# Kernel optimization log

Measured on AMD Instinct MI355X. Metric: run time of the kernel, lower is better.

Reference implementation:

```python
import jax, jax.numpy as jnp
import numpy as np

NUM_GRAPHS = 128
EPS = 1e-5  # torch BatchNorm1d default eps


def setup_inputs() -> dict:
    key = jax.random.key(0)
    ks = jax.random.split(key, 24)
    N, E, NHE = 50000, 800000, 50000
    NODE_RAW, HEDGE_RAW, H, HH, HOUT = 92, 40, 128, 128, 256
    s = 0.05
    inp = {
        "x": jax.random.normal(ks[0], (N, NODE_RAW), jnp.float32),
        "hedge_attrs": jax.random.normal(ks[1], (NHE, HEDGE_RAW), jnp.float32),
        "inter_relations_index": jax.random.randint(ks[2], (3, E), 0, N, jnp.int64),
        "batch": jax.random.randint(ks[3], (N,), 0, NUM_GRAPHS, jnp.int64),
        "num_nodes": N,
        # embed: Linear(92, h_dim)
        "embed_w": jax.random.normal(ks[4], (NODE_RAW, H), jnp.float32) * s,
        "embed_b": jax.random.normal(ks[5], (H,), jnp.float32) * s,
        # bembed: Linear(hedge_dim, hidden_hedge_dim)
        "bembed_w": jax.random.normal(ks[6], (HEDGE_RAW, HH), jnp.float32) * s,
        "bembed_b": jax.random.normal(ks[7], (HH,), jnp.float32) * s,
        # conv.lin_full_presplit: Linear(2H+HH, 2H)
        "lin_w": jax.random.normal(ks[8], (2 * H + HH, 2 * H), jnp.float32) * s,
        "lin_b": jax.random.normal(ks[9], (2 * H,), jnp.float32) * s,
        "bn1_g": jnp.ones((2 * H,), jnp.float32),
        "bn1_b": jnp.zeros((2 * H,), jnp.float32),
        "bn2_g": jnp.ones((H,), jnp.float32),
        "bn2_b": jnp.zeros((H,), jnp.float32),
        # learnable temperature of SoftmaxAggregation (init 1.0)
        "aggr_t": jnp.ones((), jnp.float32),
        "l1_w": jax.random.normal(ks[10], (H, HOUT), jnp.float32) * s,
        "l1_b": jax.random.normal(ks[11], (HOUT,), jnp.float32) * s,
        "out_w": jax.random.normal(ks[12], (HOUT, 1), jnp.float32) * s,
        "out_b": jax.random.normal(ks[13], (1,), jnp.float32) * s,
    }
    return inp


def _batchnorm(z, g, b):
    mu = z.mean(axis=0)
    var = z.var(axis=0)  # biased, matching torch training-mode normalization
    return (z - mu) * jax.lax.rsqrt(var + EPS) * g + b


def reference(x, hedge_attrs, inter_relations_index, batch, num_nodes,
              embed_w, embed_b, bembed_w, bembed_b, lin_w, lin_b,
              bn1_g, bn1_b, bn2_g, bn2_b, aggr_t, l1_w, l1_b, out_w, out_b):
    idx0 = inter_relations_index[0]
    idx1 = inter_relations_index[1]
    connect_feats = hedge_attrs @ bembed_w + bembed_b          # [NHE, HH]
    h = x @ embed_w + embed_b                                   # [N, H]

    # --- CHGInterConv ---
    origin = h[idx0]                                            # [E, H]
    connect = connect_feats[idx1]                               # [E, HH]
    remote = h[idx0]                                            # faithful to source (uses idx0)
    z = jnp.concatenate([origin, connect, remote], axis=1)      # [E, 2H+HH]
    z = z @ lin_w + lin_b                                       # [E, 2H]
    z = _batchnorm(z, bn1_g, bn1_b)
    z_f, z_c = jnp.split(z, 2, axis=-1)
    msg = jax.nn.sigmoid(z_f) * jax.nn.softplus(z_c)            # [E, H]

    # learned SoftmaxAggregation: per-node, per-channel segment softmax of t*msg
    alpha = msg * aggr_t
    m = jax.ops.segment_max(alpha, idx0, num_segments=num_nodes)
    m = jnp.where(jnp.isfinite(m), m, 0.0)                      # empty segments
    e = jnp.exp(alpha - m[idx0])
    denom = jax.ops.segment_sum(e, idx0, num_segments=num_nodes)
    w = e / (denom[idx0] + 1e-16)
    out = jax.ops.segment_sum(msg * w, idx0, num_segments=num_nodes)  # [N, H]

    out = _batchnorm(out, bn2_g, bn2_b)
    h = jax.nn.softplus(out + h)                                # residual + softplus

    # --- global mean pool over graphs ---
    counts = jax.ops.segment_sum(jnp.ones((num_nodes,), h.dtype), batch,
                                 num_segments=NUM_GRAPHS)
    pooled = jax.ops.segment_sum(h, batch, num_segments=NUM_GRAPHS)
    pooled = pooled / jnp.maximum(counts, 1.0)[:, None]         # [G, H]

    g = jax.nn.softplus(pooled @ l1_w + l1_b)                   # [G, HOUT]
    return g @ out_w + out_b                                    # [G, 1]
```

## Files before the change

kernel.cpp:

```cpp
#include <hip/hip_runtime.h>
#include <hip/hip_bf16.h>


#define EPS_BN 1e-5f
#define LOG2E 1.4426950408889634f
#define LN2   0.6931471805599453f

#define BIN_SH 8
#define BIN_CHUNK 4096

typedef __attribute__((ext_vector_type(8))) short bf16x8;
typedef __attribute__((ext_vector_type(4))) float f32x4;
typedef __attribute__((ext_vector_type(2))) float f32x2;

__device__ __forceinline__ float fexp2(float x) {
#if __has_builtin(__builtin_amdgcn_exp2f)
    return __builtin_amdgcn_exp2f(x);
#else
    return __expf(x * LN2);
#endif
}
__device__ __forceinline__ float flog2(float x) {
#if __has_builtin(__builtin_amdgcn_logf)
    return __builtin_amdgcn_logf(x);
#else
    return __logf(x) * LOG2E;
#endif
}
__device__ __forceinline__ float softplus_fast(float x) {
    return LN2 * flog2(1.f + fexp2(x * LOG2E));
}

__device__ __forceinline__ f32x2 pk_fma2(f32x2 a, f32x2 b, f32x2 c) {
#if __has_builtin(__builtin_elementwise_fma)
    return __builtin_elementwise_fma(a, b, c);
#else
    return (f32x2){fmaf(a.x, b.x, c.x), fmaf(a.y, b.y, c.y)};
#endif
}

__device__ __forceinline__ unsigned short f2bf(float f) {
    unsigned u = __float_as_uint(f);
    unsigned r = (u + 0x7fffu + ((u >> 16) & 1u)) >> 16;
    return (unsigned short)r;
}
__device__ __forceinline__ float bflo(unsigned u) { return __uint_as_float(u << 16); }
__device__ __forceinline__ float bfhi(unsigned u) { return __uint_as_float(u & 0xffff0000u); }
__device__ __forceinline__ float bfu16(unsigned short v) { return __uint_as_float(((unsigned)v) << 16); }
__device__ __forceinline__ unsigned pack2bf(float x, float y) {
    return (unsigned)f2bf(x) | ((unsigned)f2bf(y) << 16);
}

#if __has_builtin(__builtin_amdgcn_cvt_pk_f32_fp8) && __has_builtin(__builtin_amdgcn_cvt_pk_fp8_f32)
#define HW_FP8 1
#else
#define HW_FP8 0
#endif

__device__ __forceinline__ unsigned char f2fp8(float f) {
#if HW_FP8
    int r = __builtin_amdgcn_cvt_pk_fp8_f32(f, f, 0, false);
    return (unsigned char)(r & 0xff);
#else
    unsigned u = __float_as_uint(f);
    unsigned s = (u >> 24) & 0x80u;
    float af = fabsf(f);
    if (!(af >= 0.015625f)) {
        int m = (int)rintf(af * 512.f);
        if (m > 7) m = 7;
        return (unsigned char)(s | (unsigned)m);
    }
    if (af > 448.f) return (unsigned char)(s | 0x7e);
    unsigned au = __float_as_uint(af);
    unsigned r = au + 0x7ffffu + ((au >> 20) & 1u);
    int e8 = (int)(r >> 23) - 120;
    unsigned m = (r >> 20) & 7u;
    if (e8 > 15 || (e8 == 15 && m == 7)) return (unsigned char)(s | 0x7e);
    return (unsigned char)(s | ((unsigned)e8 << 3) | m);
#endif
}

__device__ __forceinline__ void fp8pair(unsigned p, f32x2& lo, f32x2& hi) {
#if HW_FP8
    lo = __builtin_amdgcn_cvt_pk_f32_fp8((int)p, false);
    hi = __builtin_amdgcn_cvt_pk_f32_fp8((int)p, true);
#else
    auto dec = [](unsigned byte) -> float {
        unsigned s = (byte & 0x80u) << 24;
        unsigned em = byte & 0x7fu;
        float nrm = __uint_as_float(s | ((em << 20) + 0x3C000000u));
        float sub = __uint_as_float(s | 0x3F800000u) * (float)em * 0.001953125f;
        return (em >= 8) ? nrm : sub;
    };
    lo = (f32x2){dec(p & 0xff), dec((p >> 8) & 0xff)};
    hi = (f32x2){dec((p >> 16) & 0xff), dec(p >> 24)};
#endif
}

__device__ __forceinline__ int perm256(int j) {
    return (j < 128) ? ((j >> 1) * 4 + (j & 1)) : (((j - 128) >> 1) * 4 + 2 + (j & 1));
}

__global__ __launch_bounds__(256) void k_prepw(const float* __restrict__ ew, const float* __restrict__ bw,
                                               const float* __restrict__ lw,
                                               unsigned short* __restrict__ embB, unsigned short* __restrict__ bembB,
                                               unsigned short* __restrict__ waB, unsigned short* __restrict__ wcB) {
    int i = blockIdx.x * 256 + threadIdx.x;
    if (i >= 81920) return;
    unsigned short* dst;
    int f, NKC, CT, mode;
    if (i < 12288)      { dst = embB;  f = i;         NKC = 3; CT = 2; mode = 0; }
    else if (i < 20480) { dst = bembB; f = i - 12288; NKC = 2; CT = 2; mode = 1; }
    else if (i < 53248) { dst = waB;   f = i - 20480; NKC = 4; CT = 4; mode = 2; }
    else                { dst = wcB;   f = i - 53248; NKC = 4; CT = 4; mode = 3; }
    int j = f & 7, l = (f >> 3) & 63;
    int r2 = f >> 9;
    int c = r2 % CT;
    int r3 = r2 / CT;
    int kc = r3 % NKC, w = r3 / NKC;
    int k = kc * 32 + ((l >> 4) & 3) * 8 + j;
    int n = (w * CT + c) * 16 + (l & 15);
    float v;
    if (mode == 0)      v = (k < 92) ? ew[k * 128 + n] : 0.f;
    else if (mode == 1) v = (k < 40) ? bw[k * 128 + n] : 0.f;
    else if (mode == 2) v = lw[k * 256 + n] + lw[(k + 256) * 256 + n];
    else                v = lw[(k + 128) * 256 + n];
    dst[f] = f2bf(v);
}

template<int KIN, int NKC1, int OMODE2>
__global__ __launch_bounds__(256) void mfma_fused(
    const float* __restrict__ in, const unsigned short* __restrict__ B1, const float* __restrict__ bias1,
    const unsigned short* __restrict__ B2, const float* __restrict__ bias2,
    unsigned short* __restrict__ hout, void* __restrict__ out2, int M,
    const int* __restrict__ aux_idx, int* __restrict__ aux_hist, int aux_cnt)
{
    const int r0 = blockIdx.x * 32;
    const int t = threadIdx.x;
    const int w = t >> 6;
    const int l = t & 63;
    const int m = l & 15, q = l >> 4;

    if (aux_idx) {
        const int T = gridDim.x * 256;
        for (int i = blockIdx.x * 256 + t; i < aux_cnt; i += T)
            atomicAdd(&aux_hist[aux_idx[i]], 1);
    }

    __shared__ __align__(16) unsigned short als[32 * NKC1 * 32];
    __shared__ __align__(16) unsigned short hls[32 * 136];

    const int KP = NKC1 * 32;
    for (int i = t; i < 32 * KP; i += 256) {
        int r = i / KP, k = i - r * KP;
        int gr = r0 + r;
        float v = (gr < M && k < KIN) ? in[(size_t)gr * KIN + k] : 0.f;
        int idx = (((r >> 4) * NKC1 + (k >> 5)) * 64 + ((k >> 3) & 3) * 16 + (r & 15)) * 8 + (k & 7);
        als[idx] = f2bf(v);
    }
    bf16x8 b1[NKC1][2];
    const bf16x8* B1f = (const bf16x8*)B1;
#pragma unroll
    for (int kc = 0; kc < NKC1; kc++)
#pragma unroll
        for (int c = 0; c < 2; c++)
            b1[kc][c] = B1f[((w * NKC1 + kc) * 2 + c) * 64 + l];
    __syncthreads();

    f32x4 acc1[2][2];
#pragma unroll
    for (int c = 0; c < 2; c++) { acc1[c][0] = (f32x4){0.f,0.f,0.f,0.f}; acc1[c][1] = (f32x4){0.f,0.f,0.f,0.f}; }
    const bf16x8* af = (const bf16x8*)als;
#pragma unroll
    for (int kc = 0; kc < NKC1; kc++) {
        bf16x8 a0 = af[kc * 64 + l];
        bf16x8 a1 = af[(NKC1 + kc) * 64 + l];
#pragma unroll
        for (int c = 0; c < 2; c++) {
            acc1[c][0] = __builtin_amdgcn_mfma_f32_16x16x32_bf16(a0, b1[kc][c], acc1[c][0], 0, 0, 0);
            acc1[c][1] = __builtin_amdgcn_mfma_f32_16x16x32_bf16(a1, b1[kc][c], acc1[c][1], 0, 0, 0);
        }
    }
#pragma unroll
    for (int c = 0; c < 2; c++) {
        int n1 = (w * 2 + c) * 16 + m;
        float bv = bias1[n1];
#pragma unroll
        for (int hh = 0; hh < 2; hh++) {
#pragma unroll
            for (int r = 0; r < 4; r++) {
                int row = hh * 16 + q * 4 + r;
                float val = acc1[c][hh][r] + bv;
                unsigned short bf = f2bf(val);
                hls[row * 136 + n1] = bf;
                if (OMODE2 == 1 && r0 + row < M) hout[(size_t)(r0 + row) * 128 + n1] = bf;
            }
        }
    }
    __syncthreads();

    bf16x8 b2[4][4];
    const bf16x8* B2f = (const bf16x8*)B2;
#pragma unroll
    for (int kc = 0; kc < 4; kc++)
#pragma unroll
        for (int c = 0; c < 4; c++)
            b2[kc][c] = B2f[((w * 4 + kc) * 4 + c) * 64 + l];

    f32x4 acc2[4][2];
#pragma unroll
    for (int c = 0; c < 4; c++) { acc2[c][0] = (f32x4){0.f,0.f,0.f,0.f}; acc2[c][1] = (f32x4){0.f,0.f,0.f,0.f}; }
#pragma unroll
    for (int kc = 0; kc < 4; kc++) {
        bf16x8 a0 = *(const bf16x8*)(hls + m * 136 + kc * 32 + q * 8);
        bf16x8 a1 = *(const bf16x8*)(hls + (m + 16) * 136 + kc * 32 + q * 8);
#pragma unroll
        for (int c = 0; c < 4; c++) {
            acc2[c][0] = __builtin_amdgcn_mfma_f32_16x16x32_bf16(a0, b2[kc][c], acc2[c][0], 0, 0, 0);
            acc2[c][1] = __builtin_amdgcn_mfma_f32_16x16x32_bf16(a1, b2[kc][c], acc2[c][1], 0, 0, 0);
        }
    }
#pragma unroll
    for (int c = 0; c < 4; c++) {
        int n = (w * 4 + c) * 16 + m;
        float bv = bias2 ? bias2[n] : 0.f;
        int pj = perm256(n);
#pragma unroll
        for (int hh = 0; hh < 2; hh++) {
#pragma unroll
            for (int r = 0; r < 4; r++) {
                int row = r0 + hh * 16 + q * 4 + r;
                if (row < M) {
                    float val = acc2[c][hh][r] + bv;
                    if (OMODE2 == 1) ((unsigned short*)out2)[(size_t)row * 256 + pj] = f2bf(val);
                    else             ((unsigned char*)out2)[(size_t)row * 256 + pj] = f2fp8(val);
                }
            }
        }
    }
}

__global__ __launch_bounds__(256) void k_count(const int* __restrict__ idx0, int* __restrict__ bsum,
                                               int E, int NB) {
    __shared__ int lhist[256];
    const int t = threadIdx.x;
    const int e0 = blockIdx.x * BIN_CHUNK;
    const int cnt = min(E - e0, BIN_CHUNK);
    lhist[t] = 0;
    __syncthreads();
    for (int i = t; i < cnt; i += 256)
        atomicAdd(&lhist[idx0[e0 + i] >> BIN_SH], 1);
    __syncthreads();
    if (t < NB && lhist[t]) atomicAdd(&bsum[t], lhist[t]);
}

__global__ __launch_bounds__(256) void k_scanB(const int* __restrict__ bsum, int* __restrict__ boff,
                                               const int* __restrict__ gcount, int* __restrict__ gptr, int NB) {
    __shared__ int s[256];
    const int t = threadIdx.x;
    int v = (t < NB) ? bsum[t] : 0;
    s[t] = v;
    __syncthreads();
#pragma unroll
    for (int ofs = 1; ofs < 256; ofs <<= 1) {
        int u = (t >= ofs) ? s[t - ofs] : 0;
        __syncthreads();
        s[t] += u;
        __syncthreads();
    }
    if (t < NB) boff[t] = s[t] - v;
    if (t == NB - 1) boff[NB] = s[t];
    __syncthreads();
    int gv = (t < 128) ? gcount[t] : 0;
    s[t] = gv;
    __syncthreads();
#pragma unroll
    for (int ofs = 1; ofs < 128; ofs <<= 1) {
        int u = (t >= ofs && t < 128) ? s[t - ofs] : 0;
        __syncthreads();
        if (t < 128) s[t] += u;
        __syncthreads();
    }
    if (t < 128) gptr[t + 1] = s[t];
    if (t == 0) gptr[0] = 0;
}

__global__ __launch_bounds__(256) void k_binA(
    const int* __restrict__ idx0, const int* __restrict__ idx1,
    const int* __restrict__ boff, int* __restrict__ bfill,
    int* __restrict__ staging,
    const int* __restrict__ batch, const int* __restrict__ gptr,
    int* __restrict__ gfill, int* __restrict__ gnodes,
    int E, int N, int NB, int EB)
{
    const int t = threadIdx.x;
    const int bid = blockIdx.x;
    if (bid >= EB) {
        int i = (bid - EB) * 256 + t;
        if (i < N) {
            int g = batch[i];
            int pos = gptr[g] + atomicAdd(&gfill[g], 1);
            gnodes[pos] = i;
        }
        return;
    }
    __shared__ int svals[BIN_CHUNK];
    __shared__ unsigned char sbk[BIN_CHUNK];
    __shared__ int lhist[256], lbase[256];
    const int e0 = bid * BIN_CHUNK;
    const int cnt = min(E - e0, BIN_CHUNK);
    for (int b = t; b < NB; b += 256) lhist[b] = 0;
    __syncthreads();
    for (int i = t; i < cnt; i += 256) {
        int n = idx0[e0 + i];
        int m = idx1[e0 + i];
        int bk = n >> BIN_SH;
        sbk[i] = (unsigned char)bk;
        svals[i] = (m << BIN_SH) | (n & ((1 << BIN_SH) - 1));
        atomicAdd(&lhist[bk], 1);
    }
    __syncthreads();
    for (int b = t; b < NB; b += 256) {
        int h = lhist[b];
        int base = h ? atomicAdd(&bfill[b], h) : 0;
        lbase[b] = boff[b] + base;
        lhist[b] = 0;
    }
    __syncthreads();
    for (int i = t; i < cnt; i += 256) {
        int bk = sbk[i];
        int r = atomicAdd(&lhist[bk], 1);
        staging[lbase[bk] + r] = svals[i];
    }
}

__global__ __launch_bounds__(256) void k_binB(
    const int* __restrict__ boff, const int* __restrict__ staging,
    int* __restrict__ rowptr, int* __restrict__ sidx1, int E, int N)
{
    __shared__ int lcnt[256];
    __shared__ int noofs[256];
    __shared__ int s[256];
    const int t = threadIdx.x;
    const int b = blockIdx.x;
    const int n0 = b << BIN_SH;
    const int nn = min(N - n0, 256);
    const int s0 = boff[b], s1 = boff[b + 1];
    lcnt[t] = 0;
    __syncthreads();
    for (int i = s0 + t; i < s1; i += 256)
        atomicAdd(&lcnt[staging[i] & 255], 1);
    __syncthreads();
    int v = lcnt[t];
    s[t] = v;
    __syncthreads();
#pragma unroll
    for (int ofs = 1; ofs < 256; ofs <<= 1) {
        int u = (t >= ofs) ? s[t - ofs] : 0;
        __syncthreads();
        s[t] += u;
        __syncthreads();
    }
    noofs[t] = s[t] - v;
    if (t < nn) rowptr[n0 + t] = s0 + s[t] - v;
    lcnt[t] = 0;
    if (b == 0 && t == 0) rowptr[N] = E;
    __syncthreads();
    for (int i = s0 + t; i < s1; i += 256) {
        int vv = staging[i];
        int nl = vv & 255;
        int r = atomicAdd(&lcnt[nl], 1);
        sidx1[s0 + noofs[nl] + r] = vv & 0xffffff00;
    }
}

__global__ __launch_bounds__(256) void k_stats(const uint2* __restrict__ A16, const unsigned char* __restrict__ Cp8b,
                                               const int* __restrict__ rowptr, const int* __restrict__ sidx1,
                                               float* __restrict__ gsum, float* __restrict__ gsq,
                                               int E, int N, int per_slot) {
    __shared__ float4 lsm4[256], lsq4[256];
    const int t = threadIdx.x;
    const int l = t & 63;
    const int wid = __builtin_amdgcn_readfirstlane(t >> 6);
    const int slot = blockIdx.x * 4 + wid;
    const unsigned lo4 = (unsigned)(l << 2);
    const long base = (long)slot * per_slot;
    const int e0 = (int)min((long)E, base);
    const int e1 = (int)min((long)E, base + per_slot);
    f32x2 smF = {0.f,0.f}, smC = {0.f,0.f};
    f32x2 sqF = {0.f,0.f}, sqC = {0.f,0.f};
    f32x2 csrF = {0.f,0.f}, csrC = {0.f,0.f};
    f32x2 aF = {0.f,0.f}, aC = {0.f,0.f};
    int cur_n = 0, bound = 0, runk = 0;

    auto flush = [&]() {
        if (runk) {
            float fk = (float)runk;
            f32x2 fk2 = {fk, fk};
            smF += csrF; smC += csrC;
            smF = pk_fma2(fk2, aF, smF);
            smC = pk_fma2(fk2, aC, smC);
            f32x2 tF = pk_fma2(fk2, aF, csrF + csrF);
            f32x2 tC = pk_fma2(fk2, aC, csrC + csrC);
            sqF = pk_fma2(aF, tF, sqF);
            sqC = pk_fma2(aC, tC, sqC);
        }
        csrF = (f32x2){0.f,0.f}; csrC = (f32x2){0.f,0.f};
        runk = 0;
    };
    auto loadA = [&](int n) {
        uint2 a8 = A16[(size_t)n * 64 + l];
        aF = (f32x2){bflo(a8.x), bfhi(a8.x)};
        aC = (f32x2){bflo(a8.y), bfhi(a8.y)};
    };

    if (e0 < e1) {
        int lo = 0, hi = N;
        while (lo + 1 < hi) {
            int mid = (lo + hi) >> 1;
            int rv = __builtin_amdgcn_readfirstlane(rowptr[mid]);
            if (rv <= e0) lo = mid; else hi = mid;
        }
        cur_n = lo;
        bound = __builtin_amdgcn_readfirstlane(rowptr[cur_n + 1]);
        loadA(cur_n);
    }

    auto proc = [&](int e, unsigned p) {
        if (e >= bound) {
            flush();
            do { cur_n++; bound = __builtin_amdgcn_readfirstlane(rowptr[cur_n + 1]); } while (bound <= e);
            loadA(cur_n);
        }
        f32x2 vf, vc;
        fp8pair(p, vf, vc);
        csrF += vf; csrC += vc;
        sqF = pk_fma2(vf, vf, sqF);
        sqC = pk_fma2(vc, vc, sqC);
        runk++;
    };

    const int nfull = (e1 - e0) & ~7;
    if (nfull > 0) {
        int eg = e0;
        unsigned cur[8];
        {
            int4 m0 = *(const int4*)(sidx1 + eg);
            int4 m1 = *(const int4*)(sidx1 + eg + 4);
            cur[0] = *(const unsigned*)(Cp8b + ((unsigned)m0.x + lo4));
            cur[1] = *(const unsigned*)(Cp8b + ((unsigned)m0.y + lo4));
            cur[2] = *(const unsigned*)(Cp8b + ((unsigned)m0.z + lo4));
            cur[3] = *(const unsigned*)(Cp8b + ((unsigned)m0.w + lo4));
            cur[4] = *(const unsigned*)(Cp8b + ((unsigned)m1.x + lo4));
            cur[5] = *(const unsigned*)(Cp8b + ((unsigned)m1.y + lo4));
            cur[6] = *(const unsigned*)(Cp8b + ((unsigned)m1.z + lo4));
            cur[7] = *(const unsigned*)(Cp8b + ((unsigned)m1.w + lo4));
        }
        for (;;) {
            const int en = eg + 8;
            const bool more = en < e0 + nfull;
            unsigned nxt[8];
            if (more) {
                int4 t0 = *(const int4*)(sidx1 + en);
                int4 t1 = *(const int4*)(sidx1 + en + 4);
                nxt[0] = *(const unsigned*)(Cp8b + ((unsigned)t0.x + lo4));
                nxt[1] = *(const unsigned*)(Cp8b + ((unsigned)t0.y + lo4));
                nxt[2] = *(const unsigned*)(Cp8b + ((unsigned)t0.z + lo4));
                nxt[3] = *(const unsigned*)(Cp8b + ((unsigned)t0.w + lo4));
                nxt[4] = *(const unsigned*)(Cp8b + ((unsigned)t1.x + lo4));
                nxt[5] = *(const unsigned*)(Cp8b + ((unsigned)t1.y + lo4));
                nxt[6] = *(const unsigned*)(Cp8b + ((unsigned)t1.z + lo4));
                nxt[7] = *(const unsigned*)(Cp8b + ((unsigned)t1.w + lo4));
            }
            proc(eg, cur[0]);     proc(eg + 1, cur[1]);
            proc(eg + 2, cur[2]); proc(eg + 3, cur[3]);
            proc(eg + 4, cur[4]); proc(eg + 5, cur[5]);
            proc(eg + 6, cur[6]); proc(eg + 7, cur[7]);
            if (!more) break;
#pragma unroll
            for (int i = 0; i < 8; i++) cur[i] = nxt[i];
            eg = en;
        }
    }
    for (int e = e0 + nfull; e < e1; e++)
        proc(e, *(const unsigned*)(Cp8b + ((unsigned)sidx1[e] + lo4)));
    flush();

    lsm4[t] = (float4){smF.x, smF.y, smC.x, smC.y};
    lsq4[t] = (float4){sqF.x, sqF.y, sqC.x, sqC.y};
    __syncthreads();
    const float* fm = (const float*)lsm4;
    const float* fq = (const float*)lsq4;
    float vs = fm[t] + fm[256 + t] + fm[512 + t] + fm[768 + t];
    float vq = fq[t] + fq[256 + t] + fq[512 + t] + fq[768 + t];
    atomicAdd(&gsum[t], vs);
    atomicAdd(&gsq[t], vq);
}

__global__ __launch_bounds__(256) void k_aggr(const uint2* __restrict__ A16, const unsigned char* __restrict__ Cp8b,
                                              const int* __restrict__ rowptr, const int* __restrict__ sidx1,
                                              const float* __restrict__ bn1_sum, const float* __restrict__ bn1_sq,
                                              const float* __restrict__ g1, const float* __restrict__ b1,
                                              const float* __restrict__ tptr, unsigned* __restrict__ out,
                                              float invE, int N) {
    const int t = threadIdx.x;
    const int l = t & 63;
    const int wid = __builtin_amdgcn_readfirstlane(t >> 6);
    const int n = blockIdx.x * 4 + wid;
    if (n >= N) return;

    const int e0 = __builtin_amdgcn_readfirstlane(rowptr[n]);
    const int e1 = __builtin_amdgcn_readfirstlane(rowptr[n + 1]);

    const float tt = tptr[0];
    const float4 sum4 = ((const float4*)bn1_sum)[l];
    const float4 sq4  = ((const float4*)bn1_sq)[l];
    const float2 gf = ((const float2*)g1)[l];
    const float2 gc = ((const float2*)(g1 + 128))[l];
    const float2 bf2 = ((const float2*)b1)[l];
    const float2 bc2 = ((const float2*)(b1 + 128))[l];
    auto mkss = [&](float sum, float sq, float gg, float bb, float& sc, float& sh) {
        float mu = sum * invE;
        float var = sq * invE - mu * mu;
        sc = gg * rsqrtf(var + EPS_BN);
        sh = fmaf(-mu, sc, bb);
    };
    float scx, shx, scy, shy, scz, shz, scw, shw;
    mkss(sum4.x, sq4.x, gf.x, bf2.x, scx, shx);
    mkss(sum4.y, sq4.y, gf.y, bf2.y, scy, shy);
    mkss(sum4.z, sq4.z, gc.x, bc2.x, scz, shz);
    mkss(sum4.w, sq4.w, gc.y, bc2.y, scw, shw);
    const f32x2 sF  = {-scx * LOG2E, -scy * LOG2E};
    const f32x2 sC  = { scz * LOG2E,  scw * LOG2E};

    uint2 a8 = A16[(size_t)n * 64 + l];
    f32x2 aF = {bflo(a8.x), bfhi(a8.x)}, aC = {bflo(a8.y), bfhi(a8.y)};
    const f32x2 bF = pk_fma2(aF, sF, (f32x2){-shx * LOG2E, -shy * LOG2E});
    const f32x2 bC = pk_fma2(aC, sC, (f32x2){ shz * LOG2E,  shw * LOG2E});

    if (e0 >= e1) { out[(size_t)n * 64 + l] = 0u; return; }

    const unsigned lo4 = (unsigned)(l << 2);
    f32x2 den = {0.f,0.f}, num = {0.f,0.f};

    auto G = [&](int e) -> unsigned {
        return *(const unsigned*)(Cp8b + ((unsigned)sidx1[e] + lo4));
    };
    auto procg = [&](unsigned p) {
        f32x2 vf, vc;
        fp8pair(p, vf, vc);
        f32x2 argf = pk_fma2(vf, sF, bF);
        f32x2 argc = pk_fma2(vc, sC, bC);
        f32x2 ef = {fexp2(argf.x), fexp2(argf.y)};
        f32x2 uu = {fexp2(argc.x), fexp2(argc.y)};
        f32x2 d1 = ef + 1.f;
        f32x2 u1 = uu + 1.f;
        f32x2 sig = {__builtin_amdgcn_rcpf(d1.x), __builtin_amdgcn_rcpf(d1.y)};
        f32x2 lg = {flog2(u1.x), flog2(u1.y)};
        f32x2 M = sig * lg;
        f32x2 tM = M * tt;
        f32x2 w = {fexp2(tM.x), fexp2(tM.y)};
        den += w;
        num = pk_fma2(M, w, num);
    };

    const int cnt = e1 - e0;
    unsigned cur[8];
#pragma unroll
    for (int i = 0; i < 8; i++)
        if (i < cnt) cur[i] = G(e0 + i);

    int e = e0;
    while (e + 8 < e1) {
        unsigned nxt[8];
#pragma unroll
        for (int i = 0; i < 8; i++)
            if (e + 8 + i < e1) nxt[i] = G(e + 8 + i);
#pragma unroll
        for (int i = 0; i < 8; i++) procg(cur[i]);
#pragma unroll
        for (int i = 0; i < 8; i++) cur[i] = nxt[i];
        e += 8;
    }
    const int rem = e1 - e;
#pragma unroll
    for (int i = 0; i < 8; i++)
        if (i < rem) procg(cur[i]);

    float ox = LN2 * num.x * __builtin_amdgcn_rcpf(den.x);
    float oy = LN2 * num.y * __builtin_amdgcn_rcpf(den.y);
    out[(size_t)n * 64 + l] = pack2bf(ox, oy);
}

__global__ __launch_bounds__(256) void k_bn2stats(const unsigned* __restrict__ outw, float* __restrict__ sum,
                                                  float* __restrict__ sq, int N) {
    __shared__ float4 ls[256];
    const int t = threadIdx.x;
    const int w = t & 63;
    const int rg = t >> 6;
    f32x2 sm = {0.f,0.f}, s2 = {0.f,0.f};
    for (int n = blockIdx.x * 4 + rg; n < N; n += gridDim.x * 4) {
        unsigned v = outw[(size_t)n * 64 + w];
        f32x2 x = {bflo(v), bfhi(v)};
        sm += x;
        s2 = pk_fma2(x, x, s2);
    }
    ls[t] = (float4){sm.x, sm.y, s2.x, s2.y};
    __syncthreads();
    if (t < 64) {
        float4 a = ls[t], b = ls[t + 64], c = ls[t + 128], d = ls[t + 192];
        atomicAdd(&sum[2 * w],     a.x + b.x + c.x + d.x);
        atomicAdd(&sum[2 * w + 1], a.y + b.y + c.y + d.y);
        atomicAdd(&sq[2 * w],      a.z + b.z + c.z + d.z);
        atomicAdd(&sq[2 * w + 1],  a.w + b.w + c.w + d.w);
    }
}

template<int SPLIT>
__global__ __launch_bounds__(128) void k_h2pool(const unsigned short* __restrict__ out,
                                                const unsigned short* __restrict__ h,
                                                const int* __restrict__ gptr, const int* __restrict__ gnodes,
                                                const float* __restrict__ bn2_sum, const float* __restrict__ bn2_sq,
                                                const float* __restrict__ g2, const float* __restrict__ b2,
                                                float* __restrict__ pooled, float invN) {
    const int g = blockIdx.x & 127;
    const int sp = blockIdx.x >> 7;
    const int c = threadIdx.x;
    float mu = bn2_sum[c] * invN;
    float var = bn2_sq[c] * invN - mu * mu;
    float sc = g2[c] * rsqrtf(var + EPS_BN);
    float sh = fmaf(-mu, sc, b2[c]);
    const int i0 = gptr[g], i1 = gptr[g + 1];
    float acc = 0.f;
    for (int i = i0 + sp; i < i1; i += SPLIT) {
        int n = gnodes[i];
        float v = fmaf(bfu16(out[(size_t)n * 128 + c]), sc, sh) + bfu16(h[(size_t)n * 128 + c]);
        acc += softplus_fast(v);
    }
    if (acc != 0.f) atomicAdd(&pooled[g * 128 + c], acc);
}

__global__ __launch_bounds__(256) void k_head(const float* __restrict__ pooled, const int* __restrict__ gcount,
                                              const float* __restrict__ l1w, const float* __restrict__ l1b,
                                              const float* __restrict__ outw, const float* __restrict__ outb,
                                              float* __restrict__ dout) {
    __shared__ float p[128];
    __shared__ float red[256];
    const int g = blockIdx.x;
    const int j = threadIdx.x;
    if (j < 128) {
        float cnt = (float)max(gcount[g], 1);
        p[j] = pooled[g * 128 + j] / cnt;
    }
    __syncthreads();
    float acc = l1b[j];
    for (int k = 0; k < 128; k++) acc = fmaf(p[k], l1w[k * 256 + j], acc);
    red[j] = softplus_fast(acc) * outw[j];
    __syncthreads();
    for (int s = 128; s > 0; s >>= 1) {
        if (j < s) red[j] += red[j + s];
        __syncthreads();
    }
    if (j == 0) dout[g] = red[0] + outb[0];
}

extern "C" void kernel_launch(void* const* d_in, const int* in_sizes, int n_in,
                              void* d_out, int out_size, void* d_ws, size_t ws_size,
                              hipStream_t stream) {
    const float* x        = (const float*)d_in[0];
    const float* hedge    = (const float*)d_in[1];
    const int*   iri      = (const int*)d_in[2];
    const int*   batch    = (const int*)d_in[3];
    const float* embed_w  = (const float*)d_in[5];
    const float* embed_b  = (const float*)d_in[6];
    const float* bembed_w = (const float*)d_in[7];
    const float* bembed_b = (const float*)d_in[8];
    const float* lin_w    = (const float*)d_in[9];
    const float* lin_b    = (const float*)d_in[10];
    const float* bn1_g    = (const float*)d_in[11];
    const float* bn1_b    = (const float*)d_in[12];
    const float* bn2_g    = (const float*)d_in[13];
    const float* bn2_b    = (const float*)d_in[14];
    const float* aggr_t   = (const float*)d_in[15];
    const float* l1_w     = (const float*)d_in[16];
    const float* l1_b     = (const float*)d_in[17];
    const float* out_w    = (const float*)d_in[18];
    const float* out_b    = (const float*)d_in[19];

    const int N   = in_sizes[0] / 92;
    const int NHE = in_sizes[1] / 40;
    const int E   = in_sizes[2] / 3;
    const int* idx0 = iri;
    const int* idx1 = iri + E;

    float* ws = (float*)d_ws;
    size_t off = 0;
    auto alloc = [&](size_t elems) -> float* {
        float* p = ws + off;
        off += (elems + 63) & ~(size_t)63;
        return p;
    };
    unsigned short* h16 = (unsigned short*)alloc((size_t)N * 64);
    uint2* A16    = (uint2*)alloc((size_t)N * 128);
    unsigned* Cp8 = (unsigned*)alloc((size_t)NHE * 64);
    unsigned short* embB  = (unsigned short*)alloc(6144);
    unsigned short* bembB = (unsigned short*)alloc(4096);
    unsigned short* waB   = (unsigned short*)alloc(16384);
    unsigned short* wcB   = (unsigned short*)alloc(16384);
    int*   rowptr = (int*)alloc((size_t)N + 1);
    int*   boff   = (int*)alloc(260);
    int*   sidx1  = (int*)alloc((size_t)E + 8);
    int*   staging = (int*)alloc((size_t)E + 8);
    int*   gptr   = (int*)alloc(129);
    int*   gnodes = (int*)alloc((size_t)N);
    unsigned* outbuf = (unsigned*)alloc((size_t)N * 64);
    float* zbase  = ws + off;
    int*   bsum   = (int*)alloc(256);
    int*   bfill  = (int*)alloc(256);
    int*   gfill  = (int*)alloc(128);
    float* bn1_sum = alloc(256);
    float* bn1_sq  = alloc(256);
    float* bn2_sum = alloc(128);
    float* bn2_sq  = alloc(128);
    float* pooled  = alloc(128 * 128);
    int*   gcount  = (int*)alloc(128);
    size_t zbytes = (size_t)((ws + off) - zbase) * sizeof(float);
    (void)ws_size;

    hipMemsetAsync(zbase, 0, zbytes, stream);

    k_prepw<<<320, 256, 0, stream>>>(embed_w, bembed_w, lin_w, embB, bembB, waB, wcB);
    const int mtN   = (N + 31) / 32;
    const int mtNHE = (NHE + 31) / 32;
    mfma_fused<92, 3, 1><<<mtN, 256, 0, stream>>>(x, embB, embed_b, waB, lin_b, h16, A16, N,
                                                  nullptr, nullptr, 0);
    mfma_fused<40, 2, 2><<<mtNHE, 256, 0, stream>>>(hedge, bembB, bembed_b, wcB, nullptr, nullptr, Cp8, NHE,
                                                    batch, gcount, N);

    const int NB = (N + 255) >> BIN_SH;
    const int EB = (E + BIN_CHUNK - 1) / BIN_CHUNK;
    k_count<<<EB, 256, 0, stream>>>(idx0, bsum, E, NB);
    k_scanB<<<1, 256, 0, stream>>>(bsum, boff, gcount, gptr, NB);

    const int GB = (N + 255) / 256;
    k_binA<<<EB + GB, 256, 0, stream>>>(idx0, idx1, boff, bfill, staging,
                                        batch, gptr, gfill, gnodes, E, N, NB, EB);

    k_binB<<<NB, 256, 0, stream>>>(boff, staging, rowptr, sidx1, E, N);

    const int EDGE_BLOCKS = 2048;
    const int NSLOTS = EDGE_BLOCKS * 4;
    int per_slot = ((E + NSLOTS - 1) / NSLOTS + 7) & ~7;
    k_stats<<<EDGE_BLOCKS, 256, 0, stream>>>(A16, (const unsigned char*)Cp8, rowptr, sidx1,
                                             bn1_sum, bn1_sq, E, N, per_slot);

    k_aggr<<<(N + 3) / 4, 256, 0, stream>>>(A16, (const unsigned char*)Cp8, rowptr, sidx1,
                                            bn1_sum, bn1_sq, bn1_g, bn1_b, aggr_t, outbuf,
                                            1.0f / (float)E, N);

    k_bn2stats<<<256, 256, 0, stream>>>((const unsigned*)outbuf, bn2_sum, bn2_sq, N);
    k_h2pool<16><<<128 * 16, 128, 0, stream>>>((const unsigned short*)outbuf, h16, gptr, gnodes,
                                               bn2_sum, bn2_sq, bn2_g, bn2_b, pooled, 1.0f / (float)N);

    k_head<<<128, 256, 0, stream>>>(pooled, gcount, l1_w, l1_b, out_w, out_b, (float*)d_out);
}
```

Before: 444.8 us.

## Store node outputs in graph-sorted order and precompute edge slot start nodes

Node-level outputs (h16 and the aggregation buffer) are now written at graph-sorted positions computed by a new scatter kernel. The pooling kernel can then read contiguous rows instead of gathering through a node list. The edge-bin and batch histograms move into the weight-prep kernel, and the k_count kernel is removed. k_binB now precomputes each stats slot's starting node, so k_stats no longer binary-searches rowptr. This trades scattered writes in the GEMM and aggregation kernels, plus an extra launch, for coalesced pooling reads and fewer searches.

```diff
diff --git a/kernel.cpp b/kernel.cpp
--- a/kernel.cpp
+++ b/kernel.cpp
@@ -101,11 +101,36 @@
     return (j < 128) ? ((j >> 1) * 4 + (j & 1)) : (((j - 128) >> 1) * 4 + 2 + (j & 1));
 }
 
-__global__ __launch_bounds__(256) void k_prepw(const float* __restrict__ ew, const float* __restrict__ bw,
-                                               const float* __restrict__ lw,
-                                               unsigned short* __restrict__ embB, unsigned short* __restrict__ bembB,
-                                               unsigned short* __restrict__ waB, unsigned short* __restrict__ wcB) {
-    int i = blockIdx.x * 256 + threadIdx.x;
+__global__ __launch_bounds__(256) void k_pre(const float* __restrict__ ew, const float* __restrict__ bw,
+                                             const float* __restrict__ lw,
+                                             unsigned short* __restrict__ embB, unsigned short* __restrict__ bembB,
+                                             unsigned short* __restrict__ waB, unsigned short* __restrict__ wcB,
+                                             const int* __restrict__ idx0, const int* __restrict__ batch,
+                                             int* __restrict__ bsum, int* __restrict__ gcount,
+                                             int E, int N, int NB) {
+    const int t = threadIdx.x;
+    const int bid = blockIdx.x;
+    if (bid >= 320) {
+        __shared__ int lhist[256];
+        __shared__ int lbat[128];
+        const int cb = bid - 320;
+        lhist[t] = 0;
+        if (t < 128) lbat[t] = 0;
+        __syncthreads();
+        const int e0 = cb * BIN_CHUNK;
+        const int ecnt = min(E - e0, BIN_CHUNK);
+        for (int i = t; i < ecnt; i += 256)
+            atomicAdd(&lhist[idx0[e0 + i] >> BIN_SH], 1);
+        const int n0 = cb * BIN_CHUNK;
+        const int ncnt = min(N - n0, BIN_CHUNK);
+        for (int i = t; i < ncnt; i += 256)
+            atomicAdd(&lbat[batch[n0 + i]], 1);
+        __syncthreads();
+        if (t < NB && lhist[t]) atomicAdd(&bsum[t], lhist[t]);
+        if (t < 128 && lbat[t]) atomicAdd(&gcount[t], lbat[t]);
+        return;
+    }
+    int i = bid * 256 + t;
     if (i >= 81920) return;
     unsigned short* dst;
     int f, NKC, CT, mode;
@@ -128,24 +153,58 @@
     dst[f] = f2bf(v);
 }
 
+__global__ __launch_bounds__(256) void k_scanB(const int* __restrict__ bsum, int* __restrict__ boff,
+                                               const int* __restrict__ gcount, int* __restrict__ gptr, int NB) {
+    __shared__ int s[256];
+    const int t = threadIdx.x;
+    int v = (t < NB) ? bsum[t] : 0;
+    s[t] = v;
+    __syncthreads();
+#pragma unroll
+    for (int ofs = 1; ofs < 256; ofs <<= 1) {
+        int u = (t >= ofs) ? s[t - ofs] : 0;
+        __syncthreads();
+        s[t] += u;
+        __syncthreads();
+    }
+    if (t < NB) boff[t] = s[t] - v;
+    if (t == NB - 1) boff[NB] = s[t];
+    __syncthreads();
+    int gv = (t < 128) ? gcount[t] : 0;
+    s[t] = gv;
+    __syncthreads();
+#pragma unroll
+    for (int ofs = 1; ofs < 128; ofs <<= 1) {
+        int u = (t >= ofs && t < 128) ? s[t - ofs] : 0;
+        __syncthreads();
+        if (t < 128) s[t] += u;
+        __syncthreads();
+    }
+    if (t < 128) gptr[t + 1] = s[t];
+    if (t == 0) gptr[0] = 0;
+}
+
+__global__ __launch_bounds__(256) void k_scatterpos(const int* __restrict__ batch, const int* __restrict__ gptr,
+                                                    int* __restrict__ gfill, int* __restrict__ pos_of, int N) {
+    int i = blockIdx.x * 256 + threadIdx.x;
+    if (i < N) {
+        int g = batch[i];
+        pos_of[i] = gptr[g] + atomicAdd(&gfill[g], 1);
+    }
+}
+
 template<int KIN, int NKC1, int OMODE2>
 __global__ __launch_bounds__(256) void mfma_fused(
     const float* __restrict__ in, const unsigned short* __restrict__ B1, const float* __restrict__ bias1,
     const unsigned short* __restrict__ B2, const float* __restrict__ bias2,
     unsigned short* __restrict__ hout, void* __restrict__ out2, int M,
-    const int* __restrict__ aux_idx, int* __restrict__ aux_hist, int aux_cnt)
+    const int* __restrict__ pos_of)
 {
     const int r0 = blockIdx.x * 32;
     const int t = threadIdx.x;
     const int w = t >> 6;
     const int l = t & 63;
     const int m = l & 15, q = l >> 4;
-
-    if (aux_idx) {
-        const int T = gridDim.x * 256;
-        for (int i = blockIdx.x * 256 + t; i < aux_cnt; i += T)
-            atomicAdd(&aux_hist[aux_idx[i]], 1);
-    }
 
     __shared__ __align__(16) unsigned short als[32 * NKC1 * 32];
     __shared__ __align__(16) unsigned short hls[32 * 136];
@@ -193,7 +252,8 @@
                 float val = acc1[c][hh][r] + bv;
                 unsigned short bf = f2bf(val);
                 hls[row * 136 + n1] = bf;
-                if (OMODE2 == 1 && r0 + row < M) hout[(size_t)(r0 + row) * 128 + n1] = bf;
+                if (OMODE2 == 1 && r0 + row < M)
+                    hout[(size_t)pos_of[r0 + row] * 128 + n1] = bf;
             }
         }
     }
@@ -240,70 +300,13 @@
     }
 }
 
-__global__ __launch_bounds__(256) void k_count(const int* __restrict__ idx0, int* __restrict__ bsum,
-                                               int E, int NB) {
-    __shared__ int lhist[256];
-    const int t = threadIdx.x;
-    const int e0 = blockIdx.x * BIN_CHUNK;
-    const int cnt = min(E - e0, BIN_CHUNK);
-    lhist[t] = 0;
-    __syncthreads();
-    for (int i = t; i < cnt; i += 256)
-        atomicAdd(&lhist[idx0[e0 + i] >> BIN_SH], 1);
-    __syncthreads();
-    if (t < NB && lhist[t]) atomicAdd(&bsum[t], lhist[t]);
-}
-
-__global__ __launch_bounds__(256) void k_scanB(const int* __restrict__ bsum, int* __restrict__ boff,
-                                               const int* __restrict__ gcount, int* __restrict__ gptr, int NB) {
-    __shared__ int s[256];
-    const int t = threadIdx.x;
-    int v = (t < NB) ? bsum[t] : 0;
-    s[t] = v;
-    __syncthreads();
-#pragma unroll
-    for (int ofs = 1; ofs < 256; ofs <<= 1) {
-        int u = (t >= ofs) ? s[t - ofs] : 0;
-        __syncthreads();
-        s[t] += u;
-        __syncthreads();
-    }
-    if (t < NB) boff[t] = s[t] - v;
-    if (t == NB - 1) boff[NB] = s[t];
-    __syncthreads();
-    int gv = (t < 128) ? gcount[t] : 0;
-    s[t] = gv;
-    __syncthreads();
-#pragma unroll
-    for (int ofs = 1; ofs < 128; ofs <<= 1) {
-        int u = (t >= ofs && t < 128) ? s[t - ofs] : 0;
-        __syncthreads();
-        if (t < 128) s[t] += u;
-        __syncthreads();
-    }
-    if (t < 128) gptr[t + 1] = s[t];
-    if (t == 0) gptr[0] = 0;
-}
-
 __global__ __launch_bounds__(256) void k_binA(
     const int* __restrict__ idx0, const int* __restrict__ idx1,
     const int* __restrict__ boff, int* __restrict__ bfill,
-    int* __restrict__ staging,
-    const int* __restrict__ batch, const int* __restrict__ gptr,
-    int* __restrict__ gfill, int* __restrict__ gnodes,
-    int E, int N, int NB, int EB)
+    int* __restrict__ staging, int E, int NB)
 {
     const int t = threadIdx.x;
     const int bid = blockIdx.x;
-    if (bid >= EB) {
-        int i = (bid - EB) * 256 + t;
-        if (i < N) {
-            int g = batch[i];
-            int pos = gptr[g] + atomicAdd(&gfill[g], 1);
-            gnodes[pos] = i;
-        }
-        return;
-    }
     __shared__ int svals[BIN_CHUNK];
     __shared__ unsigned char sbk[BIN_CHUNK];
     __shared__ int lhist[256], lbase[256];
@@ -336,7 +339,8 @@
 
 __global__ __launch_bounds__(256) void k_binB(
     const int* __restrict__ boff, const int* __restrict__ staging,
-    int* __restrict__ rowptr, int* __restrict__ sidx1, int E, int N)
+    int* __restrict__ rowptr, int* __restrict__ sidx1, int* __restrict__ slots,
+    int E, int N, int per_slot)
 {
     __shared__ int lcnt[256];
     __shared__ int noofs[256];
@@ -366,6 +370,19 @@
     lcnt[t] = 0;
     if (b == 0 && t == 0) rowptr[N] = E;
     __syncthreads();
+    if (s1 > s0) {
+        int sfirst = (s0 + per_slot - 1) / per_slot;
+        int slast  = (s1 - 1) / per_slot;
+        for (int si = sfirst + t; si <= slast; si += 256) {
+            int tgt = si * per_slot - s0;
+            int lo = 0, hi = nn;
+            while (lo + 1 < hi) {
+                int mid = (lo + hi) >> 1;
+                if (noofs[mid] <= tgt) lo = mid; else hi = mid;
+            }
+            slots[si] = n0 + lo;
+        }
+    }
     for (int i = s0 + t; i < s1; i += 256) {
         int vv = staging[i];
         int nl = vv & 255;
@@ -376,6 +393,7 @@
 
 __global__ __launch_bounds__(256) void k_stats(const uint2* __restrict__ A16, const unsigned char* __restrict__ Cp8b,
                                                const int* __restrict__ rowptr, const int* __restrict__ sidx1,
+                                               const int* __restrict__ slots,
                                                float* __restrict__ gsum, float* __restrict__ gsq,
                                                int E, int N, int per_slot) {
     __shared__ float4 lsm4[256], lsq4[256];
@@ -415,13 +433,7 @@
     };
 
     if (e0 < e1) {
-        int lo = 0, hi = N;
-        while (lo + 1 < hi) {
-            int mid = (lo + hi) >> 1;
-            int rv = __builtin_amdgcn_readfirstlane(rowptr[mid]);
-            if (rv <= e0) lo = mid; else hi = mid;
-        }
-        cur_n = lo;
+        cur_n = __builtin_amdgcn_readfirstlane(slots[slot]);
         bound = __builtin_amdgcn_readfirstlane(rowptr[cur_n + 1]);
         loadA(cur_n);
     }
@@ -499,6 +511,7 @@
 
 __global__ __launch_bounds__(256) void k_aggr(const uint2* __restrict__ A16, const unsigned char* __restrict__ Cp8b,
                                               const int* __restrict__ rowptr, const int* __restrict__ sidx1,
+                                              const int* __restrict__ pos_of,
                                               const float* __restrict__ bn1_sum, const float* __restrict__ bn1_sq,
                                               const float* __restrict__ g1, const float* __restrict__ b1,
                                               const float* __restrict__ tptr, unsigned* __restrict__ out,
@@ -511,6 +524,7 @@
 
     const int e0 = __builtin_amdgcn_readfirstlane(rowptr[n]);
     const int e1 = __builtin_amdgcn_readfirstlane(rowptr[n + 1]);
+    const int pn = __builtin_amdgcn_readfirstlane(pos_of[n]);
 
     const float tt = tptr[0];
     const float4 sum4 = ((const float4*)bn1_sum)[l];
@@ -538,7 +552,7 @@
     const f32x2 bF = pk_fma2(aF, sF, (f32x2){-shx * LOG2E, -shy * LOG2E});
     const f32x2 bC = pk_fma2(aC, sC, (f32x2){ shz * LOG2E,  shw * LOG2E});
 
-    if (e0 >= e1) { out[(size_t)n * 64 + l] = 0u; return; }
+    if (e0 >= e1) { out[(size_t)pn * 64 + l] = 0u; return; }
 
     const unsigned lo4 = (unsigned)(l << 2);
     f32x2 den = {0.f,0.f}, num = {0.f,0.f};
@@ -589,7 +603,7 @@
 
     float ox = LN2 * num.x * __builtin_amdgcn_rcpf(den.x);
     float oy = LN2 * num.y * __builtin_amdgcn_rcpf(den.y);
-    out[(size_t)n * 64 + l] = pack2bf(ox, oy);
+    out[(size_t)pn * 64 + l] = pack2bf(ox, oy);
 }
 
 __global__ __launch_bounds__(256) void k_bn2stats(const unsigned* __restrict__ outw, float* __restrict__ sum,
@@ -619,7 +633,7 @@
 template<int SPLIT>
 __global__ __launch_bounds__(128) void k_h2pool(const unsigned short* __restrict__ out,
                                                 const unsigned short* __restrict__ h,
-                                                const int* __restrict__ gptr, const int* __restrict__ gnodes,
+                                                const int* __restrict__ gptr,
                                                 const float* __restrict__ bn2_sum, const float* __restrict__ bn2_sq,
                                                 const float* __restrict__ g2, const float* __restrict__ b2,
                                                 float* __restrict__ pooled, float invN) {
@@ -633,8 +647,7 @@
     const int i0 = gptr[g], i1 = gptr[g + 1];
     float acc = 0.f;
     for (int i = i0 + sp; i < i1; i += SPLIT) {
-        int n = gnodes[i];
-        float v = fmaf(bfu16(out[(size_t)n * 128 + c]), sc, sh) + bfu16(h[(size_t)n * 128 + c]);
+        float v = fmaf(bfu16(out[(size_t)i * 128 + c]), sc, sh) + bfu16(h[(size_t)i * 128 + c]);
         acc += softplus_fast(v);
     }
     if (acc != 0.f) atomicAdd(&pooled[g * 128 + c], acc);
@@ -712,54 +725,53 @@
     int*   sidx1  = (int*)alloc((size_t)E + 8);
     int*   staging = (int*)alloc((size_t)E + 8);
     int*   gptr   = (int*)alloc(129);
-    int*   gnodes = (int*)alloc((size_t)N);
+    int*   pos_of = (int*)alloc((size_t)N);
+    int*   slots  = (int*)alloc(8200);
     unsigned* outbuf = (unsigned*)alloc((size_t)N * 64);
     float* zbase  = ws + off;
     int*   bsum   = (int*)alloc(256);
     int*   bfill  = (int*)alloc(256);
     int*   gfill  = (int*)alloc(128);
+    int*   gcount = (int*)alloc(128);
     float* bn1_sum = alloc(256);
     float* bn1_sq  = alloc(256);
     float* bn2_sum = alloc(128);
     float* bn2_sq  = alloc(128);
     float* pooled  = alloc(128 * 128);
-    int*   gcount  = (int*)alloc(128);
     size_t zbytes = (size_t)((ws + off) - zbase) * sizeof(float);
     (void)ws_size;
 
     hipMemsetAsync(zbase, 0, zbytes, stream);
 
-    k_prepw<<<320, 256, 0, stream>>>(embed_w, bembed_w, lin_w, embB, bembB, waB, wcB);
+    const int NB = (N + 255) >> BIN_SH;
+    const int EB = (E + BIN_CHUNK - 1) / BIN_CHUNK;
+
+    k_pre<<<320 + EB, 256, 0, stream>>>(embed_w, bembed_w, lin_w, embB, bembB, waB, wcB,
+                                        idx0, batch, bsum, gcount, E, N, NB);
+    k_scanB<<<1, 256, 0, stream>>>(bsum, boff, gcount, gptr, NB);
+    k_scatterpos<<<(N + 255) / 256, 256, 0, stream>>>(batch, gptr, gfill, pos_of, N);
+
     const int mtN   = (N + 31) / 32;
     const int mtNHE = (NHE + 31) / 32;
-    mfma_fused<92, 3, 1><<<mtN, 256, 0, stream>>>(x, embB, embed_b, waB, lin_b, h16, A16, N,
-                                                  nullptr, nullptr, 0);
+    mfma_fused<92, 3, 1><<<mtN, 256, 0, stream>>>(x, embB, embed_b, waB, lin_b, h16, A16, N, pos_of);
     mfma_fused<40, 2, 2><<<mtNHE, 256, 0, stream>>>(hedge, bembB, bembed_b, wcB, nullptr, nullptr, Cp8, NHE,
-                                                    batch, gcount, N);
-
-    const int NB = (N + 255) >> BIN_SH;
-    const int EB = (E + BIN_CHUNK - 1) / BIN_CHUNK;
-    k_count<<<EB, 256, 0, stream>>>(idx0, bsum, E, NB);
-    k_scanB<<<1, 256, 0, stream>>>(bsum, boff, gcount, gptr, NB);
-
-    const int GB = (N + 255) / 256;
-    k_binA<<<EB + GB, 256, 0, stream>>>(idx0, idx1, boff, bfill, staging,
-                                        batch, gptr, gfill, gnodes, E, N, NB, EB);
-
-    k_binB<<<NB, 256, 0, stream>>>(boff, staging, rowptr, sidx1, E, N);
+                                                    nullptr);
 
     const int EDGE_BLOCKS = 2048;
     const int NSLOTS = EDGE_BLOCKS * 4;
     int per_slot = ((E + NSLOTS - 1) / NSLOTS + 7) & ~7;
-    k_stats<<<EDGE_BLOCKS, 256, 0, stream>>>(A16, (const unsigned char*)Cp8, rowptr, sidx1,
+    k_binA<<<EB, 256, 0, stream>>>(idx0, idx1, boff, bfill, staging, E, NB);
+    k_binB<<<NB, 256, 0, stream>>>(boff, staging, rowptr, sidx1, slots, E, N, per_slot);
+
+    k_stats<<<EDGE_BLOCKS, 256, 0, stream>>>(A16, (const unsigned char*)Cp8, rowptr, sidx1, slots,
                                              bn1_sum, bn1_sq, E, N, per_slot);
 
-    k_aggr<<<(N + 3) / 4, 256, 0, stream>>>(A16, (const unsigned char*)Cp8, rowptr, sidx1,
+    k_aggr<<<(N + 3) / 4, 256, 0, stream>>>(A16, (const unsigned char*)Cp8, rowptr, sidx1, pos_of,
                                             bn1_sum, bn1_sq, bn1_g, bn1_b, aggr_t, outbuf,
                                             1.0f / (float)E, N);
 
     k_bn2stats<<<256, 256, 0, stream>>>((const unsigned*)outbuf, bn2_sum, bn2_sq, N);
-    k_h2pool<16><<<128 * 16, 128, 0, stream>>>((const unsigned short*)outbuf, h16, gptr, gnodes,
+    k_h2pool<16><<<128 * 16, 128, 0, stream>>>((const unsigned short*)outbuf, h16, gptr,
                                                bn2_sum, bn2_sq, bn2_g, bn2_b, pooled, 1.0f / (float)N);
 
     k_head<<<128, 256, 0, stream>>>(pooled, gcount, l1_w, l1_b, out_w, out_b, (float*)d_out);
```

Result: faster. 411.4 us (-7.5%).
